# Kernel optimization log

Measured on AMD Instinct MI355X. Metric: run time of the kernel, lower is better.

The kernel has to match this reference:

```python
import jax, jax.numpy as jnp
import numpy as np

HIDDEN = 512
INPUT_DIM = 512

def setup_inputs() -> dict:
    key = jax.random.key(0)
    ks = jax.random.split(key, 7)
    stdv = 1.0 / np.sqrt(HIDDEN)
    inp = {
        "input": jax.random.normal(ks[0], (2048, 64, INPUT_DIM), dtype=jnp.float32),
        "h_prev": jax.random.normal(ks[1], (64, HIDDEN), dtype=jnp.float32),
        "c_prev": jax.random.normal(ks[2], (64, HIDDEN), dtype=jnp.float32),
        "weight_ih": jax.random.uniform(ks[3], (4 * HIDDEN, INPUT_DIM), minval=-stdv, maxval=stdv, dtype=jnp.float32),
        "weight_hh": jax.random.uniform(ks[4], (4 * HIDDEN, HIDDEN), minval=-stdv, maxval=stdv, dtype=jnp.float32),
        "bias_ih": jax.random.uniform(ks[5], (4 * HIDDEN,), minval=-stdv, maxval=stdv, dtype=jnp.float32),
        "bias_hh": jax.random.uniform(ks[6], (4 * HIDDEN,), minval=-stdv, maxval=stdv, dtype=jnp.float32),
    }
    return inp

def reference(input, h_prev, c_prev, weight_ih, weight_hh, bias_ih, bias_hh):
    H = weight_hh.shape[1]
    # Precompute input projection for all timesteps: (S, B, 4H)
    x_proj = jnp.einsum('sbi,gi->sbg', input, weight_ih) + bias_ih + bias_hh

    def step(carry, xp):
        h, c = carry
        linear = xp + h @ weight_hh.T  # (B, 4H)
        i_t = jax.nn.sigmoid(linear[:, 0*H:1*H])
        f_t = jax.nn.sigmoid(linear[:, 1*H:2*H])
        g_t = jnp.tanh(linear[:, 2*H:3*H])
        o_t = jax.nn.sigmoid(linear[:, 3*H:4*H])
        c_t = f_t * c + i_t * g_t
        h_t = o_t * jnp.tanh(c_t)
        return (h_t, c_t), h_t

    (h_f, c_f), output = jax.lax.scan(step, (h_prev, c_prev), x_proj)
    return output, (h_f, c_f)
```

## Files before the change

kernel.cpp:

```cpp
#include <hip/hip_runtime.h>

typedef unsigned short u16;
typedef short bf16x8 __attribute__((ext_vector_type(8)));
typedef float f32x4 __attribute__((ext_vector_type(4)));

#define SS 2048
#define BB 64
#define HH 512
#define GG 2048

#define WB_ELEMS (2048 * 1024)
#define OFF_BIAS ((size_t)WB_ELEMS * 2)
#define OFF_H0   (OFF_BIAS + 2048 * 4)
#define OFF_H1   (OFF_H0 + 32768 * 2)
#define OFF_CNT  (OFF_H1 + 32768 * 2)
#define WS_BASE  (OFF_CNT + 512)
#define OFF_XBF  WS_BASE
#define WS_XBF   (OFF_XBF + (size_t)SS * BB * 512 * 2)

__device__ __forceinline__ u16 f2bf(float f) {
    unsigned int u = __builtin_bit_cast(unsigned int, f);
    u += 0x7FFFu + ((u >> 16) & 1u);
    return (u16)(u >> 16);
}

__device__ __forceinline__ bf16x8 pack8(float4 fa, float4 fb) {
    union { unsigned u[4]; bf16x8 v; } r;
    asm("v_cvt_pk_bf16_f32 %0, %1, %2" : "=v"(r.u[0]) : "v"(fa.x), "v"(fa.y));
    asm("v_cvt_pk_bf16_f32 %0, %1, %2" : "=v"(r.u[1]) : "v"(fa.z), "v"(fa.w));
    asm("v_cvt_pk_bf16_f32 %0, %1, %2" : "=v"(r.u[2]) : "v"(fb.x), "v"(fb.y));
    asm("v_cvt_pk_bf16_f32 %0, %1, %2" : "=v"(r.u[3]) : "v"(fb.z), "v"(fb.w));
    return r.v;
}

__device__ __forceinline__ void load_coh_b128(bf16x8* dst, const void* p) {
    asm volatile("global_load_dwordx4 %0, %1, off sc0 sc1" : "=v"(*dst) : "v"(p));
}

__global__ __launch_bounds__(256) void lstm_prep(
    const float* __restrict__ Wih, const float* __restrict__ Whh,
    const float* __restrict__ bih, const float* __restrict__ bhh,
    const float* __restrict__ h_prev,
    u16* __restrict__ WB, float* __restrict__ bias_p,
    u16* __restrict__ h0, unsigned* __restrict__ cnts)
{
    int idx = blockIdx.x * 256 + threadIdx.x;
    if (idx < WB_ELEMS) {
        int j    = idx & 7;
        int lane = (idx >> 3) & 63;
        int kc   = (idx >> 9) & 31;
        int gt   = idx >> 14;
        int p = gt * 16 + (lane & 15);
        int k = kc * 32 + (lane >> 4) * 8 + j;
        int q = (p >> 2) & 3;
        int h = (p >> 4) * 4 + (p & 3);
        int row = q * 512 + h;
        float v = (k < 512) ? Wih[row * 512 + k] : Whh[row * 512 + (k - 512)];
        WB[idx] = f2bf(v);
    } else if (idx < WB_ELEMS + 2048) {
        int p = idx - WB_ELEMS;
        int q = (p >> 2) & 3;
        int h = (p >> 4) * 4 + (p & 3);
        int row = q * 512 + h;
        bias_p[p] = bih[row] + bhh[row];
    } else if (idx < WB_ELEMS + 2048 + 32768) {
        int i = idx - (WB_ELEMS + 2048);
        h0[i] = f2bf(h_prev[i]);
    } else if (idx < WB_ELEMS + 2048 + 32768 + 128) {
        cnts[idx - (WB_ELEMS + 2048 + 32768)] = 0u;
    }
}

__global__ __launch_bounds__(256) void x_to_bf16(
    const float* __restrict__ x, u16* __restrict__ xb, int n8)
{
    int i = blockIdx.x * 256 + threadIdx.x;
    if (i < n8) {
        float4 fa = ((const float4*)x)[(size_t)i * 2];
        float4 fb = ((const float4*)x)[(size_t)i * 2 + 1];
        ((bf16x8*)xb)[i] = pack8(fa, fb);
    }
}

__global__ __launch_bounds__(256, 1) void lstm_persist(
    const float* __restrict__ x_all, const u16* __restrict__ xbf, int xmode,
    const u16* __restrict__ WB, const float* __restrict__ bias_p,
    const float* __restrict__ c_prev,
    u16* __restrict__ h0, u16* __restrict__ h1, unsigned* __restrict__ cnts,
    float* __restrict__ out, float* __restrict__ hf, float* __restrict__ cf)
{
    const int tid  = threadIdx.x;
    const int lane = tid & 63;
    const int wv   = tid >> 6;
    const int b    = blockIdx.x;
    const int bt   = b & 3;
    const int gt   = (b >> 2) * 4 + wv;
    const int b0   = bt * 16;
    const int col  = lane & 15;
    const int quad = lane >> 4;
    const bool qa  = (col & 4) != 0;
    const bool qb  = (col & 8) != 0;
    const int q    = col >> 2;
    const int hl   = col & 3;

    unsigned* cnt = cnts + bt * 32;

    bf16x8 wx[16], wh[16];
    {
        const u16* wb = WB + (size_t)gt * (32 * 64 * 8) + lane * 8;
#pragma unroll
        for (int kc = 0; kc < 16; ++kc) {
            wx[kc] = *(const bf16x8*)(wb + (size_t)kc * 512);
            wh[kc] = *(const bf16x8*)(wb + (size_t)(kc + 16) * 512);
        }
    }

    const float bmy = bias_p[gt * 16 + col];
    const int hid   = gt * 4 + hl;
    const int myrow = quad * 4 + q;
    const int idx   = (b0 + myrow) * 512 + hid;
    float c = c_prev[idx];

    const int ba = b0 + col;
    const u16* h0row = h0 + ba * 512 + quad * 8;
    const u16* h1row = h1 + ba * 512 + quad * 8;

    for (int t = 0; t < SS; ++t) {
        f32x4 acc = {0.f, 0.f, 0.f, 0.f};

        if (xmode) {
            const u16* xr = xbf + ((size_t)t * BB + ba) * 512 + quad * 8;
#pragma unroll
            for (int kc = 0; kc < 16; ++kc) {
                bf16x8 a = *(const bf16x8*)(xr + kc * 32);
                acc = __builtin_amdgcn_mfma_f32_16x16x32_bf16(a, wx[kc], acc, 0, 0, 0);
                if ((kc & 7) == 7) __builtin_amdgcn_sched_barrier(0);
            }
        } else {
            const float* xr = x_all + ((size_t)t * BB + ba) * 512 + quad * 8;
#pragma unroll
            for (int kc = 0; kc < 16; ++kc) {
                float4 fa = *(const float4*)(xr + kc * 32);
                float4 fb = *(const float4*)(xr + kc * 32 + 4);
                bf16x8 a = pack8(fa, fb);
                acc = __builtin_amdgcn_mfma_f32_16x16x32_bf16(a, wx[kc], acc, 0, 0, 0);
                if ((kc & 3) == 3) __builtin_amdgcn_sched_barrier(0);
            }
        }

        if (t) {
            if (tid == 0) {
                const unsigned target = 32u * (unsigned)t;
                unsigned guard = 0;
                while (__hip_atomic_load(cnt, __ATOMIC_RELAXED, __HIP_MEMORY_SCOPE_AGENT) < target) {
                    if (++guard > (1u << 24)) break;
                }
            }
            __syncthreads();
        }

        const u16* hr = ((t & 1) ? h1row : h0row);
        bf16x8 hA[16];
#pragma unroll
        for (int kc = 0; kc < 16; ++kc)
            load_coh_b128(&hA[kc], hr + kc * 32);
        asm volatile("s_waitcnt vmcnt(0)" ::: "memory");
        __builtin_amdgcn_sched_barrier(0);
#pragma unroll
        for (int kc = 0; kc < 16; ++kc)
            acc = __builtin_amdgcn_mfma_f32_16x16x32_bf16(hA[kc], wh[kc], acc, 0, 0, 0);

        float a0 = acc[0] + bmy, a1 = acc[1] + bmy, a2 = acc[2] + bmy, a3 = acc[3] + bmy;
        float s1 = qb ? (qa ? a2 : a3) : (qa ? a0 : a1);
        float s2 = qb ? (qa ? a1 : a0) : (qa ? a3 : a2);
        float s3 = qb ? (qa ? a0 : a1) : (qa ? a2 : a3);
        float v0 = qb ? (qa ? a3 : a2) : (qa ? a1 : a0);
        float v1 = __shfl_xor(s1, 4);
        float v2 = __shfl_xor(s2, 8);
        float v3 = __shfl_xor(s3, 12);
        float gi = qb ? (qa ? v3 : v2) : (qa ? v1 : v0);
        float gf = qb ? (qa ? v2 : v3) : (qa ? v0 : v1);
        float gg = qb ? (qa ? v1 : v0) : (qa ? v3 : v2);
        float go = qb ? (qa ? v0 : v1) : (qa ? v2 : v3);

        float i_ = 1.f / (1.f + __expf(-gi));
        float f_ = 1.f / (1.f + __expf(-gf));
        float g_ = 2.f / (1.f + __expf(-2.f * gg)) - 1.f;
        float o_ = 1.f / (1.f + __expf(-go));
        c = f_ * c + i_ * g_;
        float tc = 2.f / (1.f + __expf(-2.f * c)) - 1.f;
        float hnew = o_ * tc;

        u16* hout = (t & 1) ? h0 : h1;
        __hip_atomic_store(hout + idx, f2bf(hnew), __ATOMIC_RELAXED, __HIP_MEMORY_SCOPE_AGENT);
        __builtin_nontemporal_store(hnew, out + (size_t)t * (BB * HH) + idx);
        if (t == SS - 1) { hf[idx] = hnew; cf[idx] = c; }

        asm volatile("s_waitcnt vmcnt(0)" ::: "memory");
        __syncthreads();
        if (tid == 0)
            __hip_atomic_fetch_add(cnt, 1u, __ATOMIC_RELAXED, __HIP_MEMORY_SCOPE_AGENT);
    }
}

extern "C" void kernel_launch(void* const* d_in, const int* in_sizes, int n_in,
                              void* d_out, int out_size, void* d_ws, size_t ws_size,
                              hipStream_t stream) {
    const float* x      = (const float*)d_in[0];
    const float* h_prev = (const float*)d_in[1];
    const float* c_prev = (const float*)d_in[2];
    const float* Wih    = (const float*)d_in[3];
    const float* Whh    = (const float*)d_in[4];
    const float* bih    = (const float*)d_in[5];
    const float* bhh    = (const float*)d_in[6];
    float* out = (float*)d_out;

    if (ws_size < WS_BASE) return;

    char* ws = (char*)d_ws;
    u16*      WB     = (u16*)ws;
    float*    bias_p = (float*)(ws + OFF_BIAS);
    u16*      h0     = (u16*)(ws + OFF_H0);
    u16*      h1     = (u16*)(ws + OFF_H1);
    unsigned* cnts   = (unsigned*)(ws + OFF_CNT);
    u16*      xbf    = (u16*)(ws + OFF_XBF);
    int xmode = (ws_size >= WS_XBF) ? 1 : 0;

    int prep_threads = WB_ELEMS + 2048 + 32768 + 128;
    int prep_blocks = (prep_threads + 255) / 256;
    hipLaunchKernelGGL(lstm_prep, dim3(prep_blocks), dim3(256), 0, stream,
                       Wih, Whh, bih, bhh, h_prev, WB, bias_p, h0, cnts);

    if (xmode) {
        int n8 = SS * BB * 512 / 8;
        hipLaunchKernelGGL(x_to_bf16, dim3((n8 + 255) / 256), dim3(256), 0, stream,
                           x, xbf, n8);
    }

    float* hf = out + (size_t)SS * BB * HH;
    float* cf = hf + BB * HH;

    void* args[] = {
        (void*)&x, (void*)&xbf, (void*)&xmode, (void*)&WB, (void*)&bias_p,
        (void*)&c_prev, (void*)&h0, (void*)&h1, (void*)&cnts,
        (void*)&out, (void*)&hf, (void*)&cf
    };
    hipError_t err = hipLaunchCooperativeKernel(
        reinterpret_cast<void*>(lstm_persist), dim3(128), dim3(256), args, 0, stream);
    if (err != hipSuccess) {
        hipLaunchKernelGGL(lstm_persist, dim3(128), dim3(256), 0, stream,
                           x, xbf, xmode, WB, bias_p, c_prev, h0, h1, cnts, out, hf, cf);
    }
}
```

Before: 13.50 ms.

## Replace block counter barrier with per-wave step flags polled by whole wave

Each wave no longer joins a block-wide __syncthreads and a shared atomic counter. It publishes its own per-wave step flag, and every wave polls all 128 flags of its batch tile in parallel, using 64-bit lane loads combined with __all. This removes the intra-block barrier and the fetch_add contention from the recurrent critical path. The recurrent MFMA chain is split into two accumulators to shorten the dependency chain, and the output store moves after the flag publish so it is off the critical path. The cost is heavier polling traffic on the flag array and a slightly different reduction order.

```diff
diff --git a/kernel.cpp b/kernel.cpp
--- a/kernel.cpp
+++ b/kernel.cpp
@@ -13,8 +13,8 @@
 #define OFF_BIAS ((size_t)WB_ELEMS * 2)
 #define OFF_H0   (OFF_BIAS + 2048 * 4)
 #define OFF_H1   (OFF_H0 + 32768 * 2)
-#define OFF_CNT  (OFF_H1 + 32768 * 2)
-#define WS_BASE  (OFF_CNT + 512)
+#define OFF_FLG  (OFF_H1 + 32768 * 2)
+#define WS_BASE  (OFF_FLG + 2048)
 #define OFF_XBF  WS_BASE
 #define WS_XBF   (OFF_XBF + (size_t)SS * BB * 512 * 2)
 
@@ -37,12 +37,16 @@
     asm volatile("global_load_dwordx4 %0, %1, off sc0 sc1" : "=v"(*dst) : "v"(p));
 }
 
+__device__ __forceinline__ void load_pin_b128(bf16x8* dst, const void* p) {
+    asm volatile("global_load_dwordx4 %0, %1, off" : "=v"(*dst) : "v"(p));
+}
+
 __global__ __launch_bounds__(256) void lstm_prep(
     const float* __restrict__ Wih, const float* __restrict__ Whh,
     const float* __restrict__ bih, const float* __restrict__ bhh,
     const float* __restrict__ h_prev,
     u16* __restrict__ WB, float* __restrict__ bias_p,
-    u16* __restrict__ h0, unsigned* __restrict__ cnts)
+    u16* __restrict__ h0, unsigned* __restrict__ flags)
 {
     int idx = blockIdx.x * 256 + threadIdx.x;
     if (idx < WB_ELEMS) {
@@ -66,8 +70,8 @@
     } else if (idx < WB_ELEMS + 2048 + 32768) {
         int i = idx - (WB_ELEMS + 2048);
         h0[i] = f2bf(h_prev[i]);
-    } else if (idx < WB_ELEMS + 2048 + 32768 + 128) {
-        cnts[idx - (WB_ELEMS + 2048 + 32768)] = 0u;
+    } else if (idx < WB_ELEMS + 2048 + 32768 + 512) {
+        flags[idx - (WB_ELEMS + 2048 + 32768)] = 0u;
     }
 }
 
@@ -86,7 +90,7 @@
     const float* __restrict__ x_all, const u16* __restrict__ xbf, int xmode,
     const u16* __restrict__ WB, const float* __restrict__ bias_p,
     const float* __restrict__ c_prev,
-    u16* __restrict__ h0, u16* __restrict__ h1, unsigned* __restrict__ cnts,
+    u16* __restrict__ h0, u16* __restrict__ h1, unsigned* __restrict__ flags,
     float* __restrict__ out, float* __restrict__ hf, float* __restrict__ cf)
 {
     const int tid  = threadIdx.x;
@@ -103,16 +107,21 @@
     const int q    = col >> 2;
     const int hl   = col & 3;
 
-    unsigned* cnt = cnts + bt * 32;
+    unsigned* gflags = flags + bt * 128;
+    unsigned* myflag = gflags + gt;
+    const unsigned long long* pollp =
+        (const unsigned long long*)gflags + lane;
 
     bf16x8 wx[16], wh[16];
     {
         const u16* wb = WB + (size_t)gt * (32 * 64 * 8) + lane * 8;
 #pragma unroll
         for (int kc = 0; kc < 16; ++kc) {
-            wx[kc] = *(const bf16x8*)(wb + (size_t)kc * 512);
-            wh[kc] = *(const bf16x8*)(wb + (size_t)(kc + 16) * 512);
-        }
+            load_pin_b128(&wx[kc], wb + (size_t)kc * 512);
+            load_pin_b128(&wh[kc], wb + (size_t)(kc + 16) * 512);
+        }
+        asm volatile("s_waitcnt vmcnt(0)" ::: "memory");
+        __builtin_amdgcn_sched_barrier(0);
     }
 
     const float bmy = bias_p[gt * 16 + col];
@@ -126,14 +135,14 @@
     const u16* h1row = h1 + ba * 512 + quad * 8;
 
     for (int t = 0; t < SS; ++t) {
-        f32x4 acc = {0.f, 0.f, 0.f, 0.f};
+        f32x4 accX = {0.f, 0.f, 0.f, 0.f};
 
         if (xmode) {
             const u16* xr = xbf + ((size_t)t * BB + ba) * 512 + quad * 8;
 #pragma unroll
             for (int kc = 0; kc < 16; ++kc) {
                 bf16x8 a = *(const bf16x8*)(xr + kc * 32);
-                acc = __builtin_amdgcn_mfma_f32_16x16x32_bf16(a, wx[kc], acc, 0, 0, 0);
+                accX = __builtin_amdgcn_mfma_f32_16x16x32_bf16(a, wx[kc], accX, 0, 0, 0);
                 if ((kc & 7) == 7) __builtin_amdgcn_sched_barrier(0);
             }
         } else {
@@ -143,20 +152,21 @@
                 float4 fa = *(const float4*)(xr + kc * 32);
                 float4 fb = *(const float4*)(xr + kc * 32 + 4);
                 bf16x8 a = pack8(fa, fb);
-                acc = __builtin_amdgcn_mfma_f32_16x16x32_bf16(a, wx[kc], acc, 0, 0, 0);
+                accX = __builtin_amdgcn_mfma_f32_16x16x32_bf16(a, wx[kc], accX, 0, 0, 0);
                 if ((kc & 3) == 3) __builtin_amdgcn_sched_barrier(0);
             }
         }
 
         if (t) {
-            if (tid == 0) {
-                const unsigned target = 32u * (unsigned)t;
-                unsigned guard = 0;
-                while (__hip_atomic_load(cnt, __ATOMIC_RELAXED, __HIP_MEMORY_SCOPE_AGENT) < target) {
-                    if (++guard > (1u << 24)) break;
-                }
-            }
-            __syncthreads();
+            const unsigned tgt = (unsigned)t;
+            unsigned guard = 0;
+            bool ok;
+            do {
+                unsigned long long v = __hip_atomic_load(
+                    pollp, __ATOMIC_RELAXED, __HIP_MEMORY_SCOPE_AGENT);
+                ok = ((unsigned)v >= tgt) && ((unsigned)(v >> 32) >= tgt);
+                if (++guard > (1u << 22)) break;
+            } while (!__all((int)ok));
         }
 
         const u16* hr = ((t & 1) ? h1row : h0row);
@@ -166,11 +176,18 @@
             load_coh_b128(&hA[kc], hr + kc * 32);
         asm volatile("s_waitcnt vmcnt(0)" ::: "memory");
         __builtin_amdgcn_sched_barrier(0);
-#pragma unroll
-        for (int kc = 0; kc < 16; ++kc)
-            acc = __builtin_amdgcn_mfma_f32_16x16x32_bf16(hA[kc], wh[kc], acc, 0, 0, 0);
-
-        float a0 = acc[0] + bmy, a1 = acc[1] + bmy, a2 = acc[2] + bmy, a3 = acc[3] + bmy;
+        f32x4 accA = {0.f, 0.f, 0.f, 0.f};
+        f32x4 accB = {0.f, 0.f, 0.f, 0.f};
+#pragma unroll
+        for (int kc = 0; kc < 16; kc += 2) {
+            accA = __builtin_amdgcn_mfma_f32_16x16x32_bf16(hA[kc],     wh[kc],     accA, 0, 0, 0);
+            accB = __builtin_amdgcn_mfma_f32_16x16x32_bf16(hA[kc + 1], wh[kc + 1], accB, 0, 0, 0);
+        }
+
+        float a0 = accX[0] + accA[0] + accB[0] + bmy;
+        float a1 = accX[1] + accA[1] + accB[1] + bmy;
+        float a2 = accX[2] + accA[2] + accB[2] + bmy;
+        float a3 = accX[3] + accA[3] + accB[3] + bmy;
         float s1 = qb ? (qa ? a2 : a3) : (qa ? a0 : a1);
         float s2 = qb ? (qa ? a1 : a0) : (qa ? a3 : a2);
         float s3 = qb ? (qa ? a0 : a1) : (qa ? a2 : a3);
@@ -193,13 +210,10 @@
 
         u16* hout = (t & 1) ? h0 : h1;
         __hip_atomic_store(hout + idx, f2bf(hnew), __ATOMIC_RELAXED, __HIP_MEMORY_SCOPE_AGENT);
-        __builtin_nontemporal_store(hnew, out + (size_t)t * (BB * HH) + idx);
+        asm volatile("s_waitcnt vmcnt(0)" ::: "memory");
+        __hip_atomic_store(myflag, (unsigned)(t + 1), __ATOMIC_RELAXED, __HIP_MEMORY_SCOPE_AGENT);
+        out[(size_t)t * (BB * HH) + idx] = hnew;
         if (t == SS - 1) { hf[idx] = hnew; cf[idx] = c; }
-
-        asm volatile("s_waitcnt vmcnt(0)" ::: "memory");
-        __syncthreads();
-        if (tid == 0)
-            __hip_atomic_fetch_add(cnt, 1u, __ATOMIC_RELAXED, __HIP_MEMORY_SCOPE_AGENT);
     }
 }
 
@@ -222,14 +236,14 @@
     float*    bias_p = (float*)(ws + OFF_BIAS);
     u16*      h0     = (u16*)(ws + OFF_H0);
     u16*      h1     = (u16*)(ws + OFF_H1);
-    unsigned* cnts   = (unsigned*)(ws + OFF_CNT);
+    unsigned* flags  = (unsigned*)(ws + OFF_FLG);
     u16*      xbf    = (u16*)(ws + OFF_XBF);
     int xmode = (ws_size >= WS_XBF) ? 1 : 0;
 
-    int prep_threads = WB_ELEMS + 2048 + 32768 + 128;
+    int prep_threads = WB_ELEMS + 2048 + 32768 + 512;
     int prep_blocks = (prep_threads + 255) / 256;
     hipLaunchKernelGGL(lstm_prep, dim3(prep_blocks), dim3(256), 0, stream,
-                       Wih, Whh, bih, bhh, h_prev, WB, bias_p, h0, cnts);
+                       Wih, Whh, bih, bhh, h_prev, WB, bias_p, h0, flags);
 
     if (xmode) {
         int n8 = SS * BB * 512 / 8;
@@ -242,13 +256,13 @@
 
     void* args[] = {
         (void*)&x, (void*)&xbf, (void*)&xmode, (void*)&WB, (void*)&bias_p,
-        (void*)&c_prev, (void*)&h0, (void*)&h1, (void*)&cnts,
+        (void*)&c_prev, (void*)&h0, (void*)&h1, (void*)&flags,
         (void*)&out, (void*)&hf, (void*)&cf
     };
     hipError_t err = hipLaunchCooperativeKernel(
         reinterpret_cast<void*>(lstm_persist), dim3(128), dim3(256), args, 0, stream);
     if (err != hipSuccess) {
         hipLaunchKernelGGL(lstm_persist, dim3(128), dim3(256), 0, stream,
-                           x, xbf, xmode, WB, bias_p, c_prev, h0, h1, cnts, out, hf, cf);
-    }
-}
+                           x, xbf, xmode, WB, bias_p, c_prev, h0, h1, flags, out, hf, cf);
+    }
+}
```

After: 14.33 ms. 6.1% more time.
